# Kernel tuning notes

Hardware: AMD Instinct MI355X
Metric: run time of the kernel (lower is better)

## Reference

```python
import jax, jax.numpy as jnp
import numpy as np

N_NODES = 100_000
N_EDGES = 1_600_000
HIDDEN = 32


def setup_inputs() -> dict:
    key = jax.random.key(0)
    ks = jax.random.split(key, 8)
    pos = jax.random.normal(ks[0], (N_NODES, 3), dtype=jnp.float32)
    edge_index = jax.random.randint(ks[1], (2, N_EDGES), 0, N_NODES, dtype=jnp.int64)
    batch = jnp.zeros((N_NODES,), dtype=jnp.int64)
    # layer 1 MLP: Linear(3+3 -> 32) -> ReLU -> Linear(32 -> 32)
    W1 = jax.random.normal(ks[2], (6, HIDDEN), dtype=jnp.float32) * (1.0 / np.sqrt(6))
    b1 = jnp.zeros((HIDDEN,), dtype=jnp.float32)
    W2 = jax.random.normal(ks[3], (HIDDEN, HIDDEN), dtype=jnp.float32) * (1.0 / np.sqrt(HIDDEN))
    b2 = jnp.zeros((HIDDEN,), dtype=jnp.float32)
    # layer 2 MLP: Linear(32+3 -> 32) -> ReLU -> Linear(32 -> 32)
    W3 = jax.random.normal(ks[4], (HIDDEN + 3, HIDDEN), dtype=jnp.float32) * (1.0 / np.sqrt(HIDDEN + 3))
    b3 = jnp.zeros((HIDDEN,), dtype=jnp.float32)
    W4 = jax.random.normal(ks[5], (HIDDEN, HIDDEN), dtype=jnp.float32) * (1.0 / np.sqrt(HIDDEN))
    b4 = jnp.zeros((HIDDEN,), dtype=jnp.float32)
    return {"pos": pos, "edge_index": edge_index, "batch": batch,
            "W1": W1, "b1": b1, "W2": W2, "b2": b2,
            "W3": W3, "b3": b3, "W4": W4, "b4": b4}


def _pointnet_layer(h, rel, src, dst, n_nodes, Wa, ba, Wb, bb):
    # per-edge: concat(h_j, pos_j - pos_i) -> Linear -> ReLU -> Linear, then max-scatter into i
    e = jnp.concatenate([h[src], rel], axis=-1)             # [E, in+3]
    m = jax.nn.relu(e @ Wa + ba) @ Wb + bb                  # [E, out]
    agg = jax.ops.segment_max(m, dst, num_segments=n_nodes)  # [N, out], -inf for isolated nodes
    return jnp.where(jnp.isfinite(agg), agg, 0.0)


def reference(pos, edge_index, batch, W1, b1, W2, b2, W3, b3, W4, b4):
    src = edge_index[0]  # j (source)
    dst = edge_index[1]  # i (target, aggregation index)
    n_nodes = pos.shape[0]
    rel = pos[src] - pos[dst]  # [E, 3]
    h = jax.nn.relu(_pointnet_layer(pos, rel, src, dst, n_nodes, W1, b1, W2, b2))
    h = jax.nn.relu(_pointnet_layer(h, rel, src, dst, n_nodes, W3, b3, W4, b4))
    return h
```

## Files before the change

### kernel.cpp

```cpp
#include <hip/hip_runtime.h>
#include <hip/hip_bf16.h>
#include <stdint.h>


#define BS 256
#define EBS 512
#define K1_EDGES 4096

typedef float v2f __attribute__((ext_vector_type(2)));
typedef __attribute__((ext_vector_type(8))) short bf16x8;
typedef __attribute__((ext_vector_type(16))) float f32x16;
typedef __bf16 bf16v2 __attribute__((ext_vector_type(2)));

__device__ __forceinline__ unsigned ordenc(float f) {
    unsigned u = __float_as_uint(f);
    return (u & 0x80000000u) ? ~u : (u | 0x80000000u);
}
__device__ __forceinline__ float orddec(unsigned o) {
    unsigned u = (o & 0x80000000u) ? (o ^ 0x80000000u) : ~o;
    return __uint_as_float(u);
}
#define ORD_NEG_INF 0x007FFFFFu
#define SRC_MASK 0xFFFFFu

__device__ __forceinline__ unsigned cvt2(float x, float y) {
    v2f v = {x, y};
    bf16v2 b = __builtin_convertvector(v, bf16v2);
    return __builtin_bit_cast(unsigned, b);
}
__device__ __forceinline__ float bflo(unsigned u) { return __uint_as_float(u << 16); }
__device__ __forceinline__ float bfhi(unsigned u) { return __uint_as_float(u & 0xFFFF0000u); }

__device__ __forceinline__ uint4 mk_frag(uint4 ua, float4 v0, float4 v1) {
    uint4 o;
    o.x = cvt2(fmaxf(bflo(ua.x) - v0.x, 0.0f), fmaxf(bfhi(ua.x) - v0.y, 0.0f));
    o.y = cvt2(fmaxf(bflo(ua.y) - v0.z, 0.0f), fmaxf(bfhi(ua.y) - v0.w, 0.0f));
    o.z = cvt2(fmaxf(bflo(ua.z) - v1.x, 0.0f), fmaxf(bfhi(ua.z) - v1.y, 0.0f));
    o.w = cvt2(fmaxf(bflo(ua.w) - v1.z, 0.0f), fmaxf(bfhi(ua.w) - v1.w, 0.0f));
    return o;
}

__global__ __launch_bounds__(BS) void setup_kernel(
    const int* __restrict__ ei, int E, int NRP, int* __restrict__ blockHist,
    const float* __restrict__ pos, const float* __restrict__ Wa, const float* __restrict__ ba,
    unsigned* __restrict__ Ubf, float* __restrict__ V, int N, int NB1, int NBn,
    const float* __restrict__ Wb2, const float* __restrict__ Wb4,
    unsigned* __restrict__ WbtG) {
    __shared__ int hist[1024];
    const int tid = threadIdx.x;
    const int b = blockIdx.x;
    if (b < NB1) {
        for (int r = tid; r < 1024; r += BS) hist[r] = 0;
        __syncthreads();
        const int base = b * K1_EDGES;
        const int M = min(K1_EDGES, E - base);
        for (int i = tid; i < M; i += BS) atomicAdd(&hist[ei[E + base + i] >> 7], 1);
        __syncthreads();
        for (int r = tid; r < NRP; r += BS) blockHist[b * NRP + r] = hist[r];
    } else if (b < NB1 + NBn) {
        const int n = (b - NB1) * BS + tid;
        if (n >= N) return;
        const float p[3] = {pos[3 * n], pos[3 * n + 1], pos[3 * n + 2]};
        v2f u[16], v[16];
#pragma unroll
        for (int g = 0; g < 16; ++g) {
            u[g] = *reinterpret_cast<const v2f*>(&ba[g * 2]);
            v2f z = {0.0f, 0.0f};
            v[g] = z;
        }
#pragma unroll
        for (int i = 0; i < 3; ++i) {
            const v2f f = {p[i], p[i]};
#pragma unroll
            for (int g = 0; g < 16; ++g) {
                const v2f wA = *reinterpret_cast<const v2f*>(&Wa[i * 32 + g * 2]);
                const v2f wB = *reinterpret_cast<const v2f*>(&Wa[(i + 3) * 32 + g * 2]);
                u[g] = __builtin_elementwise_fma(f, wA + wB, u[g]);
                v[g] = __builtin_elementwise_fma(f, wB, v[g]);
            }
        }
        uint4* Up = reinterpret_cast<uint4*>(Ubf + (size_t)n * 16);
        float4* Vp = reinterpret_cast<float4*>(V + (size_t)n * 32);
#pragma unroll
        for (int q = 0; q < 4; ++q) {
            uint4 o;
            o.x = cvt2(u[4 * q + 0].x, u[4 * q + 0].y);
            o.y = cvt2(u[4 * q + 1].x, u[4 * q + 1].y);
            o.z = cvt2(u[4 * q + 2].x, u[4 * q + 2].y);
            o.w = cvt2(u[4 * q + 3].x, u[4 * q + 3].y);
            Up[q] = o;
        }
#pragma unroll
        for (int q = 0; q < 8; ++q)
            Vp[q] = make_float4(v[2 * q].x, v[2 * q].y, v[2 * q + 1].x, v[2 * q + 1].y);
    } else {
        if (tid < 128) {
            const int layer = tid >> 6;
            const int t = tid & 63;
            const int lnp = t & 31;
            const int hp = t >> 5;
            const float* Wb = layer ? Wb4 : Wb2;
            unsigned* dst = WbtG + layer * 512 + t * 8;
#pragma unroll
            for (int q = 0; q < 4; ++q) {
                const int p = 4 * hp + q;
                dst[q] = cvt2(Wb[(2 * p) * 32 + lnp], Wb[(2 * p + 1) * 32 + lnp]);
                dst[4 + q] = cvt2(Wb[(2 * p + 16) * 32 + lnp], Wb[(2 * p + 17) * 32 + lnp]);
            }
        }
    }
}

__global__ __launch_bounds__(512) void off_scan_kernel(const int* __restrict__ blockHist,
                                                       int NB1, int NRP,
                                                       int* __restrict__ off,
                                                       int* __restrict__ total) {
    const int r = (blockIdx.x * 512 + threadIdx.x) >> 6;
    const int lane = threadIdx.x & 63;
    if (r >= NRP) return;
    int carry = 0;
    const int chunks = (NB1 + 63) / 64;
    for (int c = 0; c < chunks; ++c) {
        const int b = c * 64 + lane;
        const int v = (b < NB1) ? blockHist[b * NRP + r] : 0;
        int x = v;
#pragma unroll
        for (int d = 1; d < 64; d <<= 1) {
            int y = __shfl_up(x, d, 64);
            if (lane >= d) x += y;
        }
        if (b < NB1) off[b * NRP + r] = carry + (x - v);
        carry += __shfl(x, 63, 64);
    }
    if (lane == 0) total[r] = carry;
}

__global__ __launch_bounds__(1024) void range_scan_kernel(const int* __restrict__ total,
                                                          int NRP, int* __restrict__ rangeBase) {
    __shared__ int s[1024];
    const int t = threadIdx.x;
    const int v = (t < NRP) ? total[t] : 0;
    s[t] = v;
    __syncthreads();
    for (int off = 1; off < 1024; off <<= 1) {
        int add = (t >= off) ? s[t - off] : 0;
        __syncthreads();
        s[t] += add;
        __syncthreads();
    }
    if (t < NRP) rangeBase[t] = s[t] - v;
}

__global__ __launch_bounds__(BS) void bucket_scatter_kernel(
    const int* __restrict__ ei, int E, int NRP, const int* __restrict__ off,
    const int* __restrict__ rangeBase, unsigned* __restrict__ sedgeB) {
    __shared__ unsigned stage[K1_EDGES];
    __shared__ unsigned short rng[K1_EDGES];
    __shared__ unsigned short inv[K1_EDGES];
    __shared__ int hist[1024], start[1024], cursor[1024];
    __shared__ int ts[BS];
    const int tid = threadIdx.x;
    for (int r = tid; r < 1024; r += BS) hist[r] = 0;
    __syncthreads();
    const int base = blockIdx.x * K1_EDGES;
    const int M = min(K1_EDGES, E - base);
    for (int i = tid; i < M; i += BS) {
        const int src = ei[base + i];
        const int dst = ei[E + base + i];
        const int r = dst >> 7;
        stage[i] = (unsigned)src | ((unsigned)(dst & 127) << 20);
        rng[i] = (unsigned short)r;
        atomicAdd(&hist[r], 1);
    }
    __syncthreads();
    {
        const int i0 = tid * 4;
        const int l0 = hist[i0], l1 = hist[i0 + 1], l2 = hist[i0 + 2], l3 = hist[i0 + 3];
        const int tsum = l0 + l1 + l2 + l3;
        ts[tid] = tsum;
        __syncthreads();
        for (int off2 = 1; off2 < BS; off2 <<= 1) {
            int add = (tid >= off2) ? ts[tid - off2] : 0;
            __syncthreads();
            ts[tid] += add;
            __syncthreads();
        }
        const int texcl = ts[tid] - tsum;
        start[i0] = texcl;
        start[i0 + 1] = texcl + l0;
        start[i0 + 2] = texcl + l0 + l1;
        start[i0 + 3] = texcl + l0 + l1 + l2;
        cursor[i0] = start[i0];
        cursor[i0 + 1] = start[i0 + 1];
        cursor[i0 + 2] = start[i0 + 2];
        cursor[i0 + 3] = start[i0 + 3];
    }
    __syncthreads();
    for (int i = tid; i < M; i += BS) {
        const int pos = atomicAdd(&cursor[rng[i]], 1);
        inv[pos] = (unsigned short)i;
    }
    __syncthreads();
    const int* offb = off + blockIdx.x * NRP;
    for (int j = tid; j < M; j += BS) {
        const int i = inv[j];
        const int r = rng[i];
        sedgeB[rangeBase[r] + offb[r] + (j - start[r])] = stage[i];
    }
}

template <int MODE>
__global__ __launch_bounds__(EBS, 6) void edge_range_kernel(
    const unsigned* __restrict__ Ubf, const float4* __restrict__ V,
    const unsigned* __restrict__ sedgeB, const int* __restrict__ rangeBase,
    const int* __restrict__ total, const unsigned* __restrict__ WbtG,
    const float* __restrict__ bb, const float* __restrict__ pos,
    const float* __restrict__ Wa2, const float* __restrict__ ba2,
    unsigned* __restrict__ Ubf2, float* __restrict__ Vbuf2,
    float* __restrict__ out, int N) {
    __shared__ unsigned aggL[4096];
    __shared__ __align__(16) float4 vlds[1152];

    const int tid = threadIdx.x;
    const int r = blockIdx.x;
    const int base = rangeBase[r];
    const int M = total[r];
    const int last = M - 1;

    const int l = tid & 63;
    const int w = tid >> 6;
    const int half = l >> 5;
    const int ln = l & 31;

#pragma unroll
    for (int i = 0; i < 8; ++i) aggL[tid + i * EBS] = ORD_NEG_INF;

    {
        const float4* Vg = V + ((size_t)r << 10);
        const int vmax = min(1024, (N - (r << 7)) * 8);
        for (int j = tid; j < vmax; j += EBS) vlds[(j >> 3) * 9 + (j & 7)] = Vg[j];
    }

    const uint4 bu0 = *reinterpret_cast<const uint4*>(WbtG + l * 8);
    const uint4 bu1 = *reinterpret_cast<const uint4*>(WbtG + l * 8 + 4);
    const float bbn = bb[ln];
    __syncthreads();

    const int nch = (M + EBS - 1) >> 9;
    unsigned pk = 0;
    if (64 * w < M) pk = sedgeB[base + min(64 * w + l, last)];
    for (int c = 0; c < nch; ++c) {
        unsigned npk = 0;
        const int ncb = (c + 1) << 9;
        const bool nextAct = (c + 1 < nch) && (ncb + 64 * w < M);
        if (nextAct) npk = sedgeB[base + min(ncb + 64 * w + l, last)];
        if ((c << 9) + 64 * w < M) {
            const unsigned pkA = __shfl(pk, ln, 64);
            const unsigned pkB = __shfl(pk, 32 + ln, 64);
            uint4 au00, au01, au10, au11;
            {
                const uint4* Up = reinterpret_cast<const uint4*>(Ubf + (size_t)(pkA & SRC_MASK) * 16);
                const float4* Vr = &vlds[(pkA >> 20) * 9];
                au00 = mk_frag(Up[half], Vr[2 * half], Vr[2 * half + 1]);
                au01 = mk_frag(Up[2 + half], Vr[4 + 2 * half], Vr[5 + 2 * half]);
            }
            {
                const uint4* Up = reinterpret_cast<const uint4*>(Ubf + (size_t)(pkB & SRC_MASK) * 16);
                const float4* Vr = &vlds[(pkB >> 20) * 9];
                au10 = mk_frag(Up[half], Vr[2 * half], Vr[2 * half + 1]);
                au11 = mk_frag(Up[2 + half], Vr[4 + 2 * half], Vr[5 + 2 * half]);
            }

            f32x16 c0, c1;
#pragma unroll
            for (int i = 0; i < 16; ++i) {
                c0[i] = bbn;
                c1[i] = bbn;
            }
            c0 = __builtin_amdgcn_mfma_f32_32x32x16_bf16(
                __builtin_bit_cast(bf16x8, au00), __builtin_bit_cast(bf16x8, bu0), c0, 0, 0, 0);
            c0 = __builtin_amdgcn_mfma_f32_32x32x16_bf16(
                __builtin_bit_cast(bf16x8, au01), __builtin_bit_cast(bf16x8, bu1), c0, 0, 0, 0);
            c1 = __builtin_amdgcn_mfma_f32_32x32x16_bf16(
                __builtin_bit_cast(bf16x8, au10), __builtin_bit_cast(bf16x8, bu0), c1, 0, 0, 0);
            c1 = __builtin_amdgcn_mfma_f32_32x32x16_bf16(
                __builtin_bit_cast(bf16x8, au11), __builtin_bit_cast(bf16x8, bu1), c1, 0, 0, 0);

#pragma unroll
            for (int rr = 0; rr < 16; ++rr) {
                const int eo = (rr & 3) + 8 * (rr >> 2) + 4 * half;
                const int d0 = __shfl(pk, eo, 64) >> 20;
                const int d1 = __shfl(pk, 32 + eo, 64) >> 20;
                atomicMax(&aggL[(d0 << 5) | ln], ordenc(c0[rr]));
                atomicMax(&aggL[(d1 << 5) | ln], ordenc(c1[rr]));
            }
        }
        pk = npk;
    }
    __syncthreads();

    if (MODE == 0) {
        const int idx = tid * 8;
        const int node = (r << 7) + (idx >> 5);
        if (node < N) {
            float4 o0, o1;
            o0.x = fmaxf(orddec(aggL[idx + 0]), 0.0f);
            o0.y = fmaxf(orddec(aggL[idx + 1]), 0.0f);
            o0.z = fmaxf(orddec(aggL[idx + 2]), 0.0f);
            o0.w = fmaxf(orddec(aggL[idx + 3]), 0.0f);
            o1.x = fmaxf(orddec(aggL[idx + 4]), 0.0f);
            o1.y = fmaxf(orddec(aggL[idx + 5]), 0.0f);
            o1.z = fmaxf(orddec(aggL[idx + 6]), 0.0f);
            o1.w = fmaxf(orddec(aggL[idx + 7]), 0.0f);
            float4* op = reinterpret_cast<float4*>(out + (size_t)node * 32 + (idx & 31));
            op[0] = o0;
            op[1] = o1;
        }
    } else {
        const int node_l = tid >> 2;
        const int qq = tid & 3;
        const int node = (r << 7) + node_l;
        if (node < N) {
            const unsigned* row = &aggL[node_l << 5];
            float h[32];
#pragma unroll
            for (int i = 0; i < 32; ++i) h[i] = fmaxf(orddec(row[i]), 0.0f);
            const float pp[3] = {pos[3 * node], pos[3 * node + 1], pos[3 * node + 2]};
            v2f u[4], v[4];
#pragma unroll
            for (int g = 0; g < 4; ++g) {
                u[g] = *reinterpret_cast<const v2f*>(&ba2[8 * qq + 2 * g]);
                v2f z = {0.0f, 0.0f};
                v[g] = z;
            }
#pragma unroll
            for (int i = 0; i < 32; ++i) {
                const v2f f = {h[i], h[i]};
#pragma unroll
                for (int g = 0; g < 4; ++g) {
                    const v2f wv =
                        *reinterpret_cast<const v2f*>(&Wa2[i * 32 + 8 * qq + 2 * g]);
                    u[g] = __builtin_elementwise_fma(f, wv, u[g]);
                }
            }
#pragma unroll
            for (int i = 0; i < 3; ++i) {
                const v2f f = {pp[i], pp[i]};
#pragma unroll
                for (int g = 0; g < 4; ++g) {
                    const v2f wv =
                        *reinterpret_cast<const v2f*>(&Wa2[(32 + i) * 32 + 8 * qq + 2 * g]);
                    u[g] = __builtin_elementwise_fma(f, wv, u[g]);
                    v[g] = __builtin_elementwise_fma(f, wv, v[g]);
                }
            }
            uint4 o;
            o.x = cvt2(u[0].x, u[0].y);
            o.y = cvt2(u[1].x, u[1].y);
            o.z = cvt2(u[2].x, u[2].y);
            o.w = cvt2(u[3].x, u[3].y);
            reinterpret_cast<uint4*>(Ubf2 + (size_t)node * 16)[qq] = o;
            float4* Vp = reinterpret_cast<float4*>(Vbuf2 + (size_t)node * 32 + 8 * qq);
            Vp[0] = make_float4(v[0].x, v[0].y, v[1].x, v[1].y);
            Vp[1] = make_float4(v[2].x, v[2].y, v[3].x, v[3].y);
        }
    }
}

extern "C" void kernel_launch(void* const* d_in, const int* in_sizes, int n_in,
                              void* d_out, int out_size, void* d_ws, size_t ws_size,
                              hipStream_t stream) {
    const float* pos = (const float*)d_in[0];
    const int* ei = (const int*)d_in[1];
    const float* W1 = (const float*)d_in[3];
    const float* b1 = (const float*)d_in[4];
    const float* W2 = (const float*)d_in[5];
    const float* b2 = (const float*)d_in[6];
    const float* W3 = (const float*)d_in[7];
    const float* b3 = (const float*)d_in[8];
    const float* W4 = (const float*)d_in[9];
    const float* b4 = (const float*)d_in[10];

    const int E = in_sizes[1] / 2;
    const int N = in_sizes[0] / 3;
    const int n32 = N * 32;
    const int NPAD = ((N + BS - 1) / BS) * BS;
    const int NR = (N + 127) / 128;
    const int NRP = ((NR + 15) / 16) * 16;
    const int NB1 = (E + K1_EDGES - 1) / K1_EDGES;
    const int BH = NB1 * NRP;

    int* blockHist = (int*)d_ws;
    int* off = blockHist + BH;
    int* total = off + BH;
    int* rangeBase = total + NRP;
    unsigned* sedgeB = (unsigned*)(rangeBase + NRP);
    unsigned* Ubf = (unsigned*)(sedgeB + E);
    float* Vbuf = (float*)(Ubf + (size_t)NPAD * 16);
    unsigned* Ubf2 = (unsigned*)(Vbuf + n32);
    float* Vbuf2 = (float*)(Ubf2 + (size_t)NPAD * 16);
    unsigned* WbtG = (unsigned*)(Vbuf2 + n32);

    const int NBn = (N + BS - 1) / BS;

    setup_kernel<<<NB1 + NBn + 1, BS, 0, stream>>>(ei, E, NRP, blockHist, pos, W1, b1, Ubf,
                                                   Vbuf, N, NB1, NBn, W2, W4, WbtG);
    off_scan_kernel<<<(NRP * 64 + 511) / 512, 512, 0, stream>>>(blockHist, NB1, NRP, off,
                                                                total);
    range_scan_kernel<<<1, 1024, 0, stream>>>(total, NRP, rangeBase);
    bucket_scatter_kernel<<<NB1, BS, 0, stream>>>(ei, E, NRP, off, rangeBase, sedgeB);

    edge_range_kernel<1><<<NR, EBS, 0, stream>>>(Ubf, (const float4*)Vbuf, sedgeB, rangeBase,
                                                 total, WbtG, b2, pos, W3, b3, Ubf2, Vbuf2,
                                                 nullptr, N);
    edge_range_kernel<0><<<NR, EBS, 0, stream>>>(Ubf2, (const float4*)Vbuf2, sedgeB,
                                                 rangeBase, total, WbtG + 512, b4, nullptr,
                                                 nullptr, nullptr, nullptr, nullptr,
                                                 (float*)d_out, N);
}
```

Before: 211.0 us.

## Prefetch next chunk's gathered U rows and stage dst indices in LDS bytes

The edge loop now issues the global gathers of Ubf rows for the next chunk before doing the current chunk's atomics, software-pipelining gather latency with LDS atomic work, and prefetches edge packets two chunks ahead. Destination local indices are written as bytes to a per-wave LDS array and read back as packed words, replacing 32 cross-lane shuffles per chunk. This raises register pressure (extra uint4s held across iterations) under the 6-waves launch bound, and adds LDS traffic for the dst table.

```diff
diff --git a/kernel.cpp b/kernel.cpp
--- a/kernel.cpp
+++ b/kernel.cpp
@@ -220,6 +220,7 @@
     float* __restrict__ out, int N) {
     __shared__ unsigned aggL[4096];
     __shared__ __align__(16) float4 vlds[1152];
+    __shared__ unsigned dstw[8][16];
 
     const int tid = threadIdx.x;
     const int r = blockIdx.x;
@@ -247,55 +248,86 @@
     __syncthreads();
 
     const int nch = (M + EBS - 1) >> 9;
-    unsigned pk = 0;
-    if (64 * w < M) pk = sedgeB[base + min(64 * w + l, last)];
+
+    unsigned pk = 0, npk = 0, pkA = 0, pkB = 0;
+    uint4 ua0, ub0, ua1, ub1;
+    if (64 * w < M) {
+        pk = sedgeB[base + min(64 * w + l, last)];
+        pkA = __shfl(pk, ln, 64);
+        pkB = __shfl(pk, 32 + ln, 64);
+        const uint4* UpA = reinterpret_cast<const uint4*>(Ubf + (size_t)(pkA & SRC_MASK) * 16);
+        const uint4* UpB = reinterpret_cast<const uint4*>(Ubf + (size_t)(pkB & SRC_MASK) * 16);
+        ua0 = UpA[half];
+        ub0 = UpA[2 + half];
+        ua1 = UpB[half];
+        ub1 = UpB[2 + half];
+    }
+    if ((nch > 1) && (512 + 64 * w < M)) npk = sedgeB[base + min(512 + 64 * w + l, last)];
+
     for (int c = 0; c < nch; ++c) {
-        unsigned npk = 0;
-        const int ncb = (c + 1) << 9;
-        const bool nextAct = (c + 1 < nch) && (ncb + 64 * w < M);
-        if (nextAct) npk = sedgeB[base + min(ncb + 64 * w + l, last)];
-        if ((c << 9) + 64 * w < M) {
-            const unsigned pkA = __shfl(pk, ln, 64);
-            const unsigned pkB = __shfl(pk, 32 + ln, 64);
-            uint4 au00, au01, au10, au11;
-            {
-                const uint4* Up = reinterpret_cast<const uint4*>(Ubf + (size_t)(pkA & SRC_MASK) * 16);
-                const float4* Vr = &vlds[(pkA >> 20) * 9];
-                au00 = mk_frag(Up[half], Vr[2 * half], Vr[2 * half + 1]);
-                au01 = mk_frag(Up[2 + half], Vr[4 + 2 * half], Vr[5 + 2 * half]);
-            }
-            {
-                const uint4* Up = reinterpret_cast<const uint4*>(Ubf + (size_t)(pkB & SRC_MASK) * 16);
-                const float4* Vr = &vlds[(pkB >> 20) * 9];
-                au10 = mk_frag(Up[half], Vr[2 * half], Vr[2 * half + 1]);
-                au11 = mk_frag(Up[2 + half], Vr[4 + 2 * half], Vr[5 + 2 * half]);
-            }
-
-            f32x16 c0, c1;
+        const bool act = ((c << 9) + 64 * w) < M;
+        const bool nact = (c + 1 < nch) && (((c + 1) << 9) + 64 * w < M);
+
+        f32x16 c0, c1;
+        if (act) {
+            reinterpret_cast<unsigned char*>(dstw[w])[l] = (unsigned char)(pk >> 20);
+
+            const float4* VrA = &vlds[(pkA >> 20) * 9];
+            const float4* VrB = &vlds[(pkB >> 20) * 9];
 #pragma unroll
             for (int i = 0; i < 16; ++i) {
                 c0[i] = bbn;
                 c1[i] = bbn;
             }
+            uint4 au;
+            au = mk_frag(ua0, VrA[2 * half], VrA[2 * half + 1]);
             c0 = __builtin_amdgcn_mfma_f32_32x32x16_bf16(
-                __builtin_bit_cast(bf16x8, au00), __builtin_bit_cast(bf16x8, bu0), c0, 0, 0, 0);
+                __builtin_bit_cast(bf16x8, au), __builtin_bit_cast(bf16x8, bu0), c0, 0, 0, 0);
+            au = mk_frag(ub0, VrA[4 + 2 * half], VrA[5 + 2 * half]);
             c0 = __builtin_amdgcn_mfma_f32_32x32x16_bf16(
-                __builtin_bit_cast(bf16x8, au01), __builtin_bit_cast(bf16x8, bu1), c0, 0, 0, 0);
+                __builtin_bit_cast(bf16x8, au), __builtin_bit_cast(bf16x8, bu1), c0, 0, 0, 0);
+            au = mk_frag(ua1, VrB[2 * half], VrB[2 * half + 1]);
             c1 = __builtin_amdgcn_mfma_f32_32x32x16_bf16(
-                __builtin_bit_cast(bf16x8, au10), __builtin_bit_cast(bf16x8, bu0), c1, 0, 0, 0);
+                __builtin_bit_cast(bf16x8, au), __builtin_bit_cast(bf16x8, bu0), c1, 0, 0, 0);
+            au = mk_frag(ub1, VrB[4 + 2 * half], VrB[5 + 2 * half]);
             c1 = __builtin_amdgcn_mfma_f32_32x32x16_bf16(
-                __builtin_bit_cast(bf16x8, au11), __builtin_bit_cast(bf16x8, bu1), c1, 0, 0, 0);
-
-#pragma unroll
-            for (int rr = 0; rr < 16; ++rr) {
-                const int eo = (rr & 3) + 8 * (rr >> 2) + 4 * half;
-                const int d0 = __shfl(pk, eo, 64) >> 20;
-                const int d1 = __shfl(pk, 32 + eo, 64) >> 20;
-                atomicMax(&aggL[(d0 << 5) | ln], ordenc(c0[rr]));
-                atomicMax(&aggL[(d1 << 5) | ln], ordenc(c1[rr]));
-            }
+                __builtin_bit_cast(bf16x8, au), __builtin_bit_cast(bf16x8, bu1), c1, 0, 0, 0);
+        }
+
+        if (nact) {
+            pkA = __shfl(npk, ln, 64);
+            pkB = __shfl(npk, 32 + ln, 64);
+            const uint4* UpA = reinterpret_cast<const uint4*>(Ubf + (size_t)(pkA & SRC_MASK) * 16);
+            const uint4* UpB = reinterpret_cast<const uint4*>(Ubf + (size_t)(pkB & SRC_MASK) * 16);
+            ua0 = UpA[half];
+            ub0 = UpA[2 + half];
+            ua1 = UpB[half];
+            ub1 = UpB[2 + half];
         }
         pk = npk;
+        {
+            const int nncb = (c + 2) << 9;
+            npk = 0;
+            if ((c + 2 < nch) && (nncb + 64 * w < M))
+                npk = sedgeB[base + min(nncb + 64 * w + l, last)];
+        }
+
+        if (act) {
+            const unsigned* dw = dstw[w];
+#pragma unroll
+            for (int g = 0; g < 4; ++g) {
+                const unsigned p0 = dw[2 * g + half];
+                const unsigned p1 = dw[8 + 2 * g + half];
+#pragma unroll
+                for (int j = 0; j < 4; ++j) {
+                    const int rr = 4 * g + j;
+                    const int d0 = (p0 >> (8 * j)) & 0x7F;
+                    const int d1 = (p1 >> (8 * j)) & 0x7F;
+                    atomicMax(&aggL[(d0 << 5) | ln], ordenc(c0[rr]));
+                    atomicMax(&aggL[(d1 << 5) | ln], ordenc(c1[rr]));
+                }
+            }
+        }
     }
     __syncthreads();
 
```

Measured after the change: 342.3 us. 62.2% more time.
